# Kernel optimization log

Measured on AMD Instinct MI355X. Metric: run time of the kernel, lower is better.

Reference implementation:

```python
import jax, jax.numpy as jnp
import numpy as np

B, S, D = 4, 4096, 1024
H, R = 16, 256
HD = D // H  # 64

def setup_inputs() -> dict:
    key = jax.random.key(0)
    ks = jax.random.split(key, 10)
    s = 1.0 / np.sqrt(D)
    return {
        "x": jax.random.normal(ks[0], (B, S, D), dtype=jnp.float32),
        "wq": jax.random.normal(ks[1], (D, D), dtype=jnp.float32) * s,
        "bq": jnp.zeros((D,), dtype=jnp.float32),
        "wk": jax.random.normal(ks[2], (D, D), dtype=jnp.float32) * s,
        "bk": jnp.zeros((D,), dtype=jnp.float32),
        "wv": jax.random.normal(ks[3], (D, D), dtype=jnp.float32) * s,
        "bv": jnp.zeros((D,), dtype=jnp.float32),
        "wo": jax.random.normal(ks[4], (D, D), dtype=jnp.float32) * s,
        "bo": jnp.zeros((D,), dtype=jnp.float32),
        "random_features": jax.random.normal(ks[5], (H, HD, R), dtype=jnp.float32),
    }

def reference(x, wq, bq, wk, bk, wv, bv, wo, bo, random_features):
    b, s, _ = x.shape
    # projections (torch Linear: x @ W.T + b) -> [b, h, s, hd]
    def proj(w, bias):
        return (x @ w.T + bias).reshape(b, s, H, HD).transpose(0, 2, 1, 3)
    q = proj(wq, bq)
    k = proj(wk, bk)
    v = proj(wv, bv)
    # random feature maps: [b,h,s,r]
    q_prime = jnp.exp(jnp.einsum('bhsd,hdr->bhsr', q, random_features)
                      - 0.5 * jnp.sum(q * q, axis=-1, keepdims=True))
    k_prime = jnp.exp(jnp.einsum('bhsd,hdr->bhsr', k, random_features)
                      - 0.5 * jnp.sum(k * k, axis=-1, keepdims=True))
    # kv aggregation: [b,h,r,hd]
    kv_prime = jnp.einsum('bhsr,bhsd->bhrd', k_prime, v)
    attn = jnp.einsum('bhsr,bhrd->bhsd', q_prime, kv_prime)
    # normalization: [b,h,s,1]
    norm = jnp.einsum('bhsr,bhr->bhs', q_prime, jnp.sum(k_prime, axis=-2))[..., None]
    attn = attn / (norm + 1e-6)
    attn = attn.transpose(0, 2, 1, 3).reshape(b, s, D)
    return attn @ wo.T + bo
```

## Files before the change

kernel.cpp:

```cpp
#include <hip/hip_runtime.h>
#include <stdint.h>

#define B_  4
#define S_  4096
#define D_  1024
#define H_  16
#define R_  256
#define HD_ 64
#define BH_ 64
#define M_  16384
#define SPLITK_ 8

typedef uint16_t u16;
typedef __attribute__((ext_vector_type(8))) short short8;
typedef __attribute__((ext_vector_type(4))) float f32x4;
typedef __attribute__((ext_vector_type(4))) unsigned short us4;

__device__ __forceinline__ u16 f2bf(float f){
  union { float f; uint32_t u; } v; v.f = f;
  uint32_t r = v.u + 0x7FFFu + ((v.u >> 16) & 1u);
  return (u16)(r >> 16);
}
__device__ __forceinline__ float bf2f(u16 h){
  union { uint32_t u; float f; } v; v.u = ((uint32_t)h) << 16;
  return v.f;
}
__device__ __forceinline__ f32x4 mfma16(short8 a, short8 b, f32x4 c){
  return __builtin_amdgcn_mfma_f32_16x16x32_bf16(a, b, c, 0, 0, 0);
}
__device__ __forceinline__ void gl_lds16(const u16* g, u16* l){
  __builtin_amdgcn_global_load_lds((const __attribute__((address_space(1))) void*)g,
                                   (__attribute__((address_space(3))) void*)l, 16, 0, 0);
}
__device__ __forceinline__ void cvt8(const float4& a, const float4& b, short8& hi, short8& lo){
  float f[8] = {a.x,a.y,a.z,a.w,b.x,b.y,b.z,b.w};
  #pragma unroll
  for (int j=0;j<8;j++){
    u16 h = f2bf(f[j]);
    hi[j] = (short)h;
    lo[j] = (short)f2bf(f[j] - bf2f(h));
  }
}

__global__ void split_kernel(const float* __restrict__ src, u16* __restrict__ hi,
                             u16* __restrict__ lo, int n4){
  int i = blockIdx.x*blockDim.x + threadIdx.x;
  if (i >= n4) return;
  float4 f = ((const float4*)src)[i];
  float ff[4] = {f.x,f.y,f.z,f.w};
  us4 hv, lv;
  #pragma unroll
  for (int j=0;j<4;j++){
    u16 h = f2bf(ff[j]);
    hv[j] = h;
    lv[j] = f2bf(ff[j] - bf2f(h));
  }
  ((us4*)hi)[i] = hv;
  if (lo) ((us4*)lo)[i] = lv;
}

__global__ void rf_split_kernel(const float* __restrict__ rf, u16* __restrict__ rhi,
                                u16* __restrict__ rlo){
  int idx = blockIdx.x*256 + threadIdx.x;
  int d = idx & 63, r = (idx >> 6) & 255, h = idx >> 14;
  float f = rf[((size_t)h*HD_ + d)*R_ + r];
  u16 hh = f2bf(f);
  rhi[idx] = hh;
  rlo[idx] = f2bf(f - bf2f(hh));
}

__device__ __forceinline__ void rowsq(const float4& x0, const float4& x1,
                                      const float4& x2, const float4& x3,
                                      int q, float sql[4]){
  float s = x0.x*x0.x + x0.y*x0.y + x0.z*x0.z + x0.w*x0.w
          + x1.x*x1.x + x1.y*x1.y + x1.z*x1.z + x1.w*x1.w
          + x2.x*x2.x + x2.y*x2.y + x2.z*x2.z + x2.w*x2.w
          + x3.x*x3.x + x3.y*x3.y + x3.z*x3.z + x3.w*x3.w;
  s += __shfl_xor(s, 16);
  s += __shfl_xor(s, 32);
  #pragma unroll
  for (int r4=0;r4<4;r4++) sql[r4] = 0.5f * __shfl(s, q*4 + r4);
}

template<int NSPLIT, int EPI>
__global__ __launch_bounds__(256, 2)
void gemm128(const u16* __restrict__ Ah, const u16* __restrict__ Al,
             const u16* __restrict__ Bh, const u16* __restrict__ Bl,
             const float* __restrict__ bias, float* __restrict__ outF,
             u16* __restrict__ outB){
  constexpr int NBUF = (NSPLIT==3) ? 4 : 2;
  __shared__ u16 lds[NBUF * 4096];
  const int tid = threadIdx.x, w = tid >> 6, lane = tid & 63;
  const int wm = w & 1, wn = w >> 1;
  const int m0 = blockIdx.x * 128, n0 = blockIdx.y * 128;
  const int q = lane >> 4, rr = lane & 15;

  const int c0 = w*2, c1 = w*2 + 1;
  const int row0 = c0*16 + (lane >> 2), row1 = c1*16 + (lane >> 2);
  const int g0 = (lane & 3) ^ ((row0 >> 1) & 3);
  const int g1 = (lane & 3) ^ ((row1 >> 1) & 3);
  const size_t a0 = (size_t)(m0 + row0)*1024 + g0*8;
  const size_t a1 = (size_t)(m0 + row1)*1024 + g1*8;
  const size_t b0 = (size_t)(n0 + row0)*1024 + g0*8;
  const size_t b1 = (size_t)(n0 + row1)*1024 + g1*8;

  f32x4 acc[4][4];
  #pragma unroll
  for (int i=0;i<4;i++)
    #pragma unroll
    for (int j=0;j<4;j++) acc[i][j] = f32x4{0.f,0.f,0.f,0.f};

  for (int kt=0; kt<32; kt++){
    const int k0 = kt*32;
    gl_lds16(Ah + a0 + k0, lds + 0*4096 + c0*512);
    gl_lds16(Ah + a1 + k0, lds + 0*4096 + c1*512);
    gl_lds16(Bh + b0 + k0, lds + 1*4096 + c0*512);
    gl_lds16(Bh + b1 + k0, lds + 1*4096 + c1*512);
    if constexpr (NSPLIT == 3){
      gl_lds16(Al + a0 + k0, lds + 2*4096 + c0*512);
      gl_lds16(Al + a1 + k0, lds + 2*4096 + c1*512);
      gl_lds16(Bl + b0 + k0, lds + 3*4096 + c0*512);
      gl_lds16(Bl + b1 + k0, lds + 3*4096 + c1*512);
    }
    __syncthreads();

    short8 afh[4], bfh[4], afl[4], bfl[4];
    #pragma unroll
    for (int i=0;i<4;i++){
      int r  = wm*64 + i*16 + rr;
      int o  = r*32 + ((q ^ ((r >> 1) & 3))*8);
      afh[i] = *(const short8*)(lds + 0*4096 + o);
      if constexpr (NSPLIT == 3) afl[i] = *(const short8*)(lds + 2*4096 + o);
      int rn = wn*64 + i*16 + rr;
      int on = rn*32 + ((q ^ ((rn >> 1) & 3))*8);
      bfh[i] = *(const short8*)(lds + 1*4096 + on);
      if constexpr (NSPLIT == 3) bfl[i] = *(const short8*)(lds + 3*4096 + on);
    }
    #pragma unroll
    for (int i=0;i<4;i++)
      #pragma unroll
      for (int j=0;j<4;j++){
        acc[i][j] = mfma16(afh[i], bfh[j], acc[i][j]);
        if constexpr (NSPLIT == 3){
          acc[i][j] = mfma16(afh[i], bfl[j], acc[i][j]);
          acc[i][j] = mfma16(afl[i], bfh[j], acc[i][j]);
        }
      }
    __syncthreads();
  }

  #pragma unroll
  for (int i=0;i<4;i++){
    #pragma unroll
    for (int j=0;j<4;j++){
      int n  = n0 + wn*64 + j*16 + rr;
      float bb = bias[n];
      if constexpr (EPI == 1){
        int mb = m0 + wm*64 + i*16 + q*4;
        us4 pk;
        #pragma unroll
        for (int r4=0;r4<4;r4++) pk[r4] = f2bf(acc[i][j][r4] + bb);
        *(us4*)(outB + ((size_t)((mb >> 12)*H_ + (n >> 6))*HD_ + (n & 63))*S_ + (mb & 4095)) = pk;
      } else {
        #pragma unroll
        for (int r4=0;r4<4;r4++){
          int m = m0 + wm*64 + i*16 + q*4 + r4;
          float v = acc[i][j][r4] + bb;
          if constexpr (EPI == 0)
            outF[((size_t)((m >> 12)*H_ + (n >> 6)))*S_*HD_ + (size_t)(m & 4095)*HD_ + (n & 63)] = v;
          else
            outF[(size_t)m*1024 + n] = v;
        }
      }
    }
  }
}

__global__ __launch_bounds__(256, 1)
void kfeat_kv_kernel(const float* __restrict__ k32,
                     const u16* __restrict__ rfh, const u16* __restrict__ rfl,
                     const u16* __restrict__ vt, u16* __restrict__ kvp16){
  __shared__ u16 kp[R_*72];
  const int sp = blockIdx.x, hb = blockIdx.y, h = hb & 15;
  const int tid = threadIdx.x, w = tid >> 6, lane = tid & 63;
  const int q = lane >> 4, rr = lane & 15;

  short8 ones;
  { u16 one = (rr == 0) ? (u16)0x3F80 : (u16)0;
    #pragma unroll
    for (int j=0;j<8;j++) ones[j] = (short)one; }

  f32x4 acc2[4][5];
  #pragma unroll
  for (int a=0;a<4;a++)
    #pragma unroll
    for (int t=0;t<5;t++) acc2[a][t] = f32x4{0.f,0.f,0.f,0.f};

  for (int sub=0; sub<(S_/SPLITK_)/64; sub++){
    const int s0 = sp*(S_/SPLITK_) + sub*64;
    const float* ap = k32 + ((size_t)hb*S_ + s0 + w*16 + rr)*HD_ + q*8;
    float4 x0 = *(const float4*)(ap);
    float4 x1 = *(const float4*)(ap + 4);
    float4 x2 = *(const float4*)(ap + 32);
    float4 x3 = *(const float4*)(ap + 36);
    float sql[4];
    rowsq(x0, x1, x2, x3, q, sql);
    short8 ah[2], al[2];
    cvt8(x0, x1, ah[0], al[0]);
    cvt8(x2, x3, ah[1], al[1]);

    f32x4 accp[16];
    #pragma unroll
    for (int t=0;t<16;t++) accp[t] = f32x4{0.f,0.f,0.f,0.f};
    #pragma unroll
    for (int t=0;t<16;t++){
      const u16* bp  = rfh + ((size_t)h*R_ + t*16 + rr)*HD_ + q*8;
      const u16* bpl = rfl + ((size_t)h*R_ + t*16 + rr)*HD_ + q*8;
      short8 bh0 = *(const short8*)(bp);
      short8 bh1 = *(const short8*)(bp + 32);
      short8 bl0 = *(const short8*)(bpl);
      short8 bl1 = *(const short8*)(bpl + 32);
      f32x4 c = accp[t];
      c = mfma16(ah[0], bh0, c); c = mfma16(ah[0], bl0, c); c = mfma16(al[0], bh0, c);
      c = mfma16(ah[1], bh1, c); c = mfma16(ah[1], bl1, c); c = mfma16(al[1], bh1, c);
      accp[t] = c;
    }
    #pragma unroll
    for (int t=0;t<16;t++){
      us4 pk;
      #pragma unroll
      for (int r4=0;r4<4;r4++) pk[r4] = f2bf(__expf(accp[t][r4] - sql[r4]));
      *(us4*)(kp + (t*16 + rr)*72 + w*16 + q*4) = pk;
    }
    __syncthreads();
    #pragma unroll
    for (int ks=0; ks<2; ks++){
      short8 af[4];
      #pragma unroll
      for (int a=0;a<4;a++)
        af[a] = *(const short8*)(kp + (w*64 + a*16 + rr)*72 + ks*32 + q*8);
      #pragma unroll
      for (int t=0;t<5;t++){
        short8 bf;
        if (t < 4)
          bf = *(const short8*)(vt + ((size_t)hb*HD_ + t*16 + rr)*S_ + s0 + ks*32 + q*8);
        else
          bf = ones;
        #pragma unroll
        for (int a=0;a<4;a++) acc2[a][t] = mfma16(af[a], bf, acc2[a][t]);
      }
    }
    __syncthreads();
  }
  u16* op = kvp16 + ((size_t)hb*SPLITK_ + sp)*R_*80;
  #pragma unroll
  for (int a=0;a<4;a++)
    #pragma unroll
    for (int t=0;t<5;t++)
      #pragma unroll
      for (int r4=0;r4<4;r4++){
        int r = w*64 + a*16 + q*4 + r4;
        int c = t*16 + rr;
        op[r*80 + c] = f2bf(acc2[a][t][r4]);
      }
}

__global__ void kv_reduce_kernel(const u16* __restrict__ kvp16, u16* __restrict__ kvt,
                                 float* __restrict__ ksum){
  int r = blockIdx.x, hb = blockIdx.y, c = threadIdx.x;
  if (c >= 65) return;
  const u16* base = kvp16 + (size_t)hb*SPLITK_*R_*80 + r*80 + c;
  float s = 0.f;
  #pragma unroll
  for (int sp=0; sp<SPLITK_; sp++) s += bf2f(base[(size_t)sp*R_*80]);
  if (c < 64) kvt[((size_t)hb*HD_ + c)*R_ + r] = f2bf(s);
  else        ksum[(size_t)hb*R_ + r] = s;
}

__global__ __launch_bounds__(256, 1)
void qfeat_attn_kernel(const float* __restrict__ q32,
                       const u16* __restrict__ rfh, const u16* __restrict__ rfl,
                       const u16* __restrict__ kvt, const float* __restrict__ ksum,
                       u16* __restrict__ attn_c){
  __shared__ u16 qp[64*264];
  const int sc4 = blockIdx.x, hb = blockIdx.y, h = hb & 15, b = hb >> 4;
  const int tid = threadIdx.x, w = tid >> 6, lane = tid & 63;
  const int q = lane >> 4, rr = lane & 15;

  float kslv[16];
  #pragma unroll
  for (int t=0;t<16;t++) kslv[t] = ksum[(size_t)hb*R_ + t*16 + rr];

  for (int sub=0; sub<4; sub++){
    const int s0 = sc4*256 + sub*64;
    const float* ap = q32 + ((size_t)hb*S_ + s0 + w*16 + rr)*HD_ + q*8;
    float4 x0 = *(const float4*)(ap);
    float4 x1 = *(const float4*)(ap + 4);
    float4 x2 = *(const float4*)(ap + 32);
    float4 x3 = *(const float4*)(ap + 36);
    float sql[4];
    rowsq(x0, x1, x2, x3, q, sql);
    short8 ah[2], al[2];
    cvt8(x0, x1, ah[0], al[0]);
    cvt8(x2, x3, ah[1], al[1]);

    f32x4 accp[16];
    #pragma unroll
    for (int t=0;t<16;t++) accp[t] = f32x4{0.f,0.f,0.f,0.f};
    #pragma unroll
    for (int t=0;t<16;t++){
      const u16* bp  = rfh + ((size_t)h*R_ + t*16 + rr)*HD_ + q*8;
      const u16* bpl = rfl + ((size_t)h*R_ + t*16 + rr)*HD_ + q*8;
      short8 bh0 = *(const short8*)(bp);
      short8 bh1 = *(const short8*)(bp + 32);
      short8 bl0 = *(const short8*)(bpl);
      short8 bl1 = *(const short8*)(bpl + 32);
      f32x4 c = accp[t];
      c = mfma16(ah[0], bh0, c); c = mfma16(ah[0], bl0, c); c = mfma16(al[0], bh0, c);
      c = mfma16(ah[1], bh1, c); c = mfma16(ah[1], bl1, c); c = mfma16(al[1], bh1, c);
      accp[t] = c;
    }
    float npl[4] = {0.f, 0.f, 0.f, 0.f};
    #pragma unroll
    for (int t=0;t<16;t++){
      us4 pk;
      #pragma unroll
      for (int r4=0;r4<4;r4++){
        float e = __expf(accp[t][r4] - sql[r4]);
        npl[r4] += e * kslv[t];
        pk[r4] = f2bf(e);
      }
      #pragma unroll
      for (int r4=0;r4<4;r4++)
        qp[(w*16 + q*4 + r4)*264 + t*16 + rr] = pk[r4];
    }
    #pragma unroll
    for (int r4=0;r4<4;r4++){
      npl[r4] += __shfl_xor(npl[r4], 1);
      npl[r4] += __shfl_xor(npl[r4], 2);
      npl[r4] += __shfl_xor(npl[r4], 4);
      npl[r4] += __shfl_xor(npl[r4], 8);
    }
    __syncthreads();

    f32x4 acc[4];
    #pragma unroll
    for (int t=0;t<4;t++) acc[t] = f32x4{0.f,0.f,0.f,0.f};
    #pragma unroll
    for (int ks=0; ks<8; ks++){
      short8 af = *(const short8*)(qp + (w*16 + rr)*264 + ks*32 + q*8);
      #pragma unroll
      for (int t=0;t<4;t++){
        short8 bf = *(const short8*)(kvt + ((size_t)hb*HD_ + t*16 + rr)*R_ + ks*32 + q*8);
        acc[t] = mfma16(af, bf, acc[t]);
      }
    }

    #pragma unroll
    for (int t=0;t<4;t++)
      #pragma unroll
      for (int r4=0;r4<4;r4++){
        int sl = w*16 + q*4 + r4;
        int d  = t*16 + rr;
        float o = acc[t][r4] / (npl[r4] + 1e-6f);
        attn_c[((size_t)b*S_ + s0 + sl)*D_ + h*HD_ + d] = f2bf(o);
      }
    __syncthreads();
  }
}

extern "C" void kernel_launch(void* const* d_in, const int* in_sizes, int n_in,
                              void* d_out, int out_size, void* d_ws, size_t ws_size,
                              hipStream_t stream){
  (void)in_sizes; (void)n_in; (void)out_size; (void)ws_size;
  const float* x  = (const float*)d_in[0];
  const float* wq = (const float*)d_in[1];
  const float* bq = (const float*)d_in[2];
  const float* wk = (const float*)d_in[3];
  const float* bk = (const float*)d_in[4];
  const float* wv = (const float*)d_in[5];
  const float* bv = (const float*)d_in[6];
  const float* wo = (const float*)d_in[7];
  const float* bo = (const float*)d_in[8];
  const float* rf = (const float*)d_in[9];
  float* out = (float*)d_out;

  char* p = (char*)d_ws;
  size_t off = 0;
  auto take = [&](size_t bytes)->char*{
    char* r = p + off; off += (bytes + 255) & ~(size_t)255; return r;
  };
  u16*  x_hi  = (u16*)take((size_t)M_*D_*2);
  u16*  x_lo  = (u16*)take((size_t)M_*D_*2);
  u16*  wq_hi = (u16*)take((size_t)D_*D_*2);
  u16*  wq_lo = (u16*)take((size_t)D_*D_*2);
  u16*  wk_hi = (u16*)take((size_t)D_*D_*2);
  u16*  wk_lo = (u16*)take((size_t)D_*D_*2);
  u16*  wv_hi = (u16*)take((size_t)D_*D_*2);
  u16*  wo_hi = (u16*)take((size_t)D_*D_*2);
  u16*  rf_hi = (u16*)take((size_t)H_*R_*HD_*2);
  u16*  rf_lo = (u16*)take((size_t)H_*R_*HD_*2);
  float* q32  = (float*)take((size_t)M_*D_*4);
  float* k32  = (float*)take((size_t)M_*D_*4);
  u16*  v_t   = (u16*)take((size_t)M_*D_*2);
  u16*  kvt   = (u16*)take((size_t)BH_*HD_*R_*2);
  float* ksum = (float*)take((size_t)BH_*R_*4);
  u16* attn_c = x_hi;
  u16* kvp16  = x_lo;

  split_kernel<<<dim3((M_*D_)/1024), 256, 0, stream>>>(x,  x_hi,  x_lo,  (M_*D_)/4);
  split_kernel<<<dim3((D_*D_)/1024), 256, 0, stream>>>(wq, wq_hi, wq_lo, (D_*D_)/4);
  split_kernel<<<dim3((D_*D_)/1024), 256, 0, stream>>>(wk, wk_hi, wk_lo, (D_*D_)/4);
  split_kernel<<<dim3((D_*D_)/1024), 256, 0, stream>>>(wv, wv_hi, nullptr, (D_*D_)/4);
  split_kernel<<<dim3((D_*D_)/1024), 256, 0, stream>>>(wo, wo_hi, nullptr, (D_*D_)/4);
  rf_split_kernel<<<dim3((H_*R_*HD_)/256), 256, 0, stream>>>(rf, rf_hi, rf_lo);

  gemm128<3,0><<<dim3(M_/128, D_/128), 256, 0, stream>>>(x_hi, x_lo, wq_hi, wq_lo, bq, q32, nullptr);
  gemm128<3,0><<<dim3(M_/128, D_/128), 256, 0, stream>>>(x_hi, x_lo, wk_hi, wk_lo, bk, k32, nullptr);
  gemm128<1,1><<<dim3(M_/128, D_/128), 256, 0, stream>>>(x_hi, nullptr, wv_hi, nullptr, bv, nullptr, v_t);

  kfeat_kv_kernel<<<dim3(SPLITK_, BH_), 256, 0, stream>>>(k32, rf_hi, rf_lo, v_t, kvp16);
  kv_reduce_kernel<<<dim3(R_, BH_), 128, 0, stream>>>(kvp16, kvt, ksum);

  qfeat_attn_kernel<<<dim3(16, BH_), 256, 0, stream>>>(q32, rf_hi, rf_lo, kvt, ksum, attn_c);

  gemm128<1,2><<<dim3(M_/128, D_/128), 256, 0, stream>>>(attn_c, nullptr, wo_hi, nullptr, bo, out, nullptr);
}
```

Before: 699.1 us.

## Stage random features in swizzled LDS and prefetch next Q/K rows

Both feature-map kernels now copy the per-head hi/lo random-feature matrices into LDS once per block, using async global-to-LDS loads with an XOR swizzle. The inner MFMA loop then reads from LDS instead of re-fetching from global memory on every sub-tile. The next 64-row slice of Q/K is loaded into registers while the current slice is computed, and the block-wide barriers in the Q attention loop are removed because each wave only touches its own rows of the shared tile. The cost is about 64KB of extra LDS per block and more register pressure.

```diff
diff --git a/kernel.cpp b/kernel.cpp
--- a/kernel.cpp
+++ b/kernel.cpp
@@ -39,6 +39,22 @@
     u16 h = f2bf(f[j]);
     hi[j] = (short)h;
     lo[j] = (short)f2bf(f[j] - bf2f(h));
+  }
+}
+
+__device__ __forceinline__ void stage_rf(const u16* __restrict__ rfh,
+                                         const u16* __restrict__ rfl,
+                                         int h, int tid, int w,
+                                         u16* lrfh, u16* lrfl){
+  const u16* baseH = rfh + (size_t)h*(R_*HD_);
+  const u16* baseL = rfl + (size_t)h*(R_*HD_);
+  #pragma unroll
+  for (int c=0;c<8;c++){
+    int idx = c*256 + tid;
+    int row = idx >> 3, gd = idx & 7;
+    int gs  = gd ^ (row & 7);
+    gl_lds16(baseH + row*64 + gs*8, lrfh + c*2048 + w*512);
+    gl_lds16(baseL + row*64 + gs*8, lrfl + c*2048 + w*512);
   }
 }
 
@@ -181,9 +197,14 @@
                      const u16* __restrict__ rfh, const u16* __restrict__ rfl,
                      const u16* __restrict__ vt, u16* __restrict__ kvp16){
   __shared__ u16 kp[R_*72];
+  __shared__ u16 lrfh[R_*HD_];
+  __shared__ u16 lrfl[R_*HD_];
   const int sp = blockIdx.x, hb = blockIdx.y, h = hb & 15;
   const int tid = threadIdx.x, w = tid >> 6, lane = tid & 63;
   const int q = lane >> 4, rr = lane & 15;
+  const int sw8 = rr & 7;
+
+  stage_rf(rfh, rfl, h, tid, w, lrfh, lrfl);
 
   short8 ones;
   { u16 one = (rr == 0) ? (u16)0x3F80 : (u16)0;
@@ -196,30 +217,40 @@
     #pragma unroll
     for (int t=0;t<5;t++) acc2[a][t] = f32x4{0.f,0.f,0.f,0.f};
 
+  __syncthreads();
+
+  const float* ap0 = k32 + ((size_t)hb*S_ + sp*(S_/SPLITK_) + w*16 + rr)*HD_ + q*8;
+  float4 x0 = *(const float4*)(ap0);
+  float4 x1 = *(const float4*)(ap0 + 4);
+  float4 x2 = *(const float4*)(ap0 + 32);
+  float4 x3 = *(const float4*)(ap0 + 36);
+
   for (int sub=0; sub<(S_/SPLITK_)/64; sub++){
     const int s0 = sp*(S_/SPLITK_) + sub*64;
-    const float* ap = k32 + ((size_t)hb*S_ + s0 + w*16 + rr)*HD_ + q*8;
-    float4 x0 = *(const float4*)(ap);
-    float4 x1 = *(const float4*)(ap + 4);
-    float4 x2 = *(const float4*)(ap + 32);
-    float4 x3 = *(const float4*)(ap + 36);
     float sql[4];
     rowsq(x0, x1, x2, x3, q, sql);
     short8 ah[2], al[2];
     cvt8(x0, x1, ah[0], al[0]);
     cvt8(x2, x3, ah[1], al[1]);
+    if (sub < (S_/SPLITK_)/64 - 1){
+      const float* apn = k32 + ((size_t)hb*S_ + s0 + 64 + w*16 + rr)*HD_ + q*8;
+      x0 = *(const float4*)(apn);
+      x1 = *(const float4*)(apn + 4);
+      x2 = *(const float4*)(apn + 32);
+      x3 = *(const float4*)(apn + 36);
+    }
 
     f32x4 accp[16];
     #pragma unroll
     for (int t=0;t<16;t++) accp[t] = f32x4{0.f,0.f,0.f,0.f};
     #pragma unroll
     for (int t=0;t<16;t++){
-      const u16* bp  = rfh + ((size_t)h*R_ + t*16 + rr)*HD_ + q*8;
-      const u16* bpl = rfl + ((size_t)h*R_ + t*16 + rr)*HD_ + q*8;
-      short8 bh0 = *(const short8*)(bp);
-      short8 bh1 = *(const short8*)(bp + 32);
-      short8 bl0 = *(const short8*)(bpl);
-      short8 bl1 = *(const short8*)(bpl + 32);
+      const u16* lrow  = lrfh + (t*16 + rr)*64;
+      const u16* lrowl = lrfl + (t*16 + rr)*64;
+      short8 bh0 = *(const short8*)(lrow  + ((q     ^ sw8))*8);
+      short8 bh1 = *(const short8*)(lrow  + (((q+4) ^ sw8))*8);
+      short8 bl0 = *(const short8*)(lrowl + ((q     ^ sw8))*8);
+      short8 bl1 = *(const short8*)(lrowl + (((q+4) ^ sw8))*8);
       f32x4 c = accp[t];
       c = mfma16(ah[0], bh0, c); c = mfma16(ah[0], bl0, c); c = mfma16(al[0], bh0, c);
       c = mfma16(ah[1], bh1, c); c = mfma16(ah[1], bl1, c); c = mfma16(al[1], bh1, c);
@@ -283,38 +314,53 @@
                        const u16* __restrict__ kvt, const float* __restrict__ ksum,
                        u16* __restrict__ attn_c){
   __shared__ u16 qp[64*264];
+  __shared__ u16 lrfh[R_*HD_];
+  __shared__ u16 lrfl[R_*HD_];
   const int sc4 = blockIdx.x, hb = blockIdx.y, h = hb & 15, b = hb >> 4;
   const int tid = threadIdx.x, w = tid >> 6, lane = tid & 63;
   const int q = lane >> 4, rr = lane & 15;
+  const int sw8 = rr & 7;
+
+  stage_rf(rfh, rfl, h, tid, w, lrfh, lrfl);
 
   float kslv[16];
   #pragma unroll
   for (int t=0;t<16;t++) kslv[t] = ksum[(size_t)hb*R_ + t*16 + rr];
+
+  __syncthreads();
+
+  const float* ap0 = q32 + ((size_t)hb*S_ + sc4*256 + w*16 + rr)*HD_ + q*8;
+  float4 x0 = *(const float4*)(ap0);
+  float4 x1 = *(const float4*)(ap0 + 4);
+  float4 x2 = *(const float4*)(ap0 + 32);
+  float4 x3 = *(const float4*)(ap0 + 36);
 
   for (int sub=0; sub<4; sub++){
     const int s0 = sc4*256 + sub*64;
-    const float* ap = q32 + ((size_t)hb*S_ + s0 + w*16 + rr)*HD_ + q*8;
-    float4 x0 = *(const float4*)(ap);
-    float4 x1 = *(const float4*)(ap + 4);
-    float4 x2 = *(const float4*)(ap + 32);
-    float4 x3 = *(const float4*)(ap + 36);
     float sql[4];
     rowsq(x0, x1, x2, x3, q, sql);
     short8 ah[2], al[2];
     cvt8(x0, x1, ah[0], al[0]);
     cvt8(x2, x3, ah[1], al[1]);
+    if (sub < 3){
+      const float* apn = q32 + ((size_t)hb*S_ + s0 + 64 + w*16 + rr)*HD_ + q*8;
+      x0 = *(const float4*)(apn);
+      x1 = *(const float4*)(apn + 4);
+      x2 = *(const float4*)(apn + 32);
+      x3 = *(const float4*)(apn + 36);
+    }
 
     f32x4 accp[16];
     #pragma unroll
     for (int t=0;t<16;t++) accp[t] = f32x4{0.f,0.f,0.f,0.f};
     #pragma unroll
     for (int t=0;t<16;t++){
-      const u16* bp  = rfh + ((size_t)h*R_ + t*16 + rr)*HD_ + q*8;
-      const u16* bpl = rfl + ((size_t)h*R_ + t*16 + rr)*HD_ + q*8;
-      short8 bh0 = *(const short8*)(bp);
-      short8 bh1 = *(const short8*)(bp + 32);
-      short8 bl0 = *(const short8*)(bpl);
-      short8 bl1 = *(const short8*)(bpl + 32);
+      const u16* lrow  = lrfh + (t*16 + rr)*64;
+      const u16* lrowl = lrfl + (t*16 + rr)*64;
+      short8 bh0 = *(const short8*)(lrow  + ((q     ^ sw8))*8);
+      short8 bh1 = *(const short8*)(lrow  + (((q+4) ^ sw8))*8);
+      short8 bl0 = *(const short8*)(lrowl + ((q     ^ sw8))*8);
+      short8 bl1 = *(const short8*)(lrowl + (((q+4) ^ sw8))*8);
       f32x4 c = accp[t];
       c = mfma16(ah[0], bh0, c); c = mfma16(ah[0], bl0, c); c = mfma16(al[0], bh0, c);
       c = mfma16(ah[1], bh1, c); c = mfma16(ah[1], bl1, c); c = mfma16(al[1], bh1, c);
@@ -341,7 +387,6 @@
       npl[r4] += __shfl_xor(npl[r4], 4);
       npl[r4] += __shfl_xor(npl[r4], 8);
     }
-    __syncthreads();
 
     f32x4 acc[4];
     #pragma unroll
@@ -365,7 +410,6 @@
         float o = acc[t][r4] / (npl[r4] + 1e-6f);
         attn_c[((size_t)b*S_ + s0 + sl)*D_ + h*HD_ + d] = f2bf(o);
       }
-    __syncthreads();
   }
 }
 
```

Measured after the change: 649.8 us. -7.0%, faster.
